# Kernel optimization log

Hardware: AMD Instinct MI355X
Metric: run time of the kernel (lower is better)

## Reference

```python
import jax, jax.numpy as jnp
import numpy as np


def setup_inputs() -> dict:
    key = jax.random.key(0)
    k1, k2 = jax.random.split(key)
    n, g, dim, cb_size = 32768, 4, 128, 512
    x = jax.random.normal(k1, (n, g, dim), dtype=jnp.float32)
    code_book = jax.random.normal(k2, (g, cb_size, dim), dtype=jnp.float32)
    return {"x": x, "code_book": code_book}


def reference(x, code_book):
    # x: (n, g, dim); code_book: (g, cb_size, dim)
    x2 = jnp.sum(x * x, axis=-1, keepdims=True)          # (n, g, 1)
    cb2 = jnp.sum(code_book * code_book, axis=-1)        # (g, cb_size)
    cross = jnp.einsum('gkd,ngd->ngk', code_book, x)     # (n, g, cb_size)
    dist = x2 + cb2 - 2.0 * cross                        # (n, g, cb_size)
    index = jnp.argmin(dist, axis=-1, keepdims=True)     # (n, g, 1) int
    one_hot = jax.nn.one_hot(index[..., 0], code_book.shape[1], dtype=dist.dtype)  # (n, g, cb_size)
    x_hat = jnp.einsum('ngk,gkd->ngd', one_hot, code_book)  # (n, g, dim)
    return (x_hat, one_hot, index)
```

## Files before the change

kernel.cpp:

```cpp
#include <hip/hip_runtime.h>
#include <hip/hip_bf16.h>

#define N_TOT 32768
#define G 4
#define DIM 128
#define CB 512
#define BM 32

#define XHAT_OFF   0
#define ONEHOT_OFF ((size_t)N_TOT * G * DIM)
#define IDX_OFF    (ONEHOT_OFF + (size_t)N_TOT * G * CB)

#define CB2_BYTES    ((size_t)G * CB * 4)
#define CBH_OFF      CB2_BYTES
#define CBHALF_BYTES ((size_t)G * CB * DIM * 2)
#define CBL_OFF      (CBH_OFF + CBHALF_BYTES)
#define WS_NEED      (CBL_OFF + CBHALF_BYTES)

typedef _Float16 half8    __attribute__((ext_vector_type(8)));
typedef _Float16 half4    __attribute__((ext_vector_type(4)));
typedef float    floatx16 __attribute__((ext_vector_type(16)));
typedef float    floatx4  __attribute__((ext_vector_type(4)));

__device__ __forceinline__ void split8(floatx4 v0, floatx4 v1, half8& hi, half8& lo) {
    float f[8] = {v0.x, v0.y, v0.z, v0.w, v1.x, v1.y, v1.z, v1.w};
#pragma unroll
    for (int e = 0; e < 8; ++e) {
        _Float16 h = (_Float16)f[e];
        hi[e] = h;
        lo[e] = (_Float16)(f[e] - (float)h);
    }
}

__global__ void cvq_cb2_kernel(const float* __restrict__ cb, float* __restrict__ cb2h) {
    int i = blockIdx.x * 256 + threadIdx.x;
    if (i >= G * CB) return;
    const float4* p = (const float4*)&cb[(size_t)i * DIM];
    float s = 0.f;
#pragma unroll
    for (int j = 0; j < DIM / 4; ++j) {
        float4 v = p[j];
        s += v.x * v.x + v.y * v.y + v.z * v.z + v.w * v.w;
    }
    cb2h[i] = 0.5f * s;
}

__global__ void cvq_cbpack_kernel(const float* __restrict__ cb,
                                  _Float16* __restrict__ cbfh, _Float16* __restrict__ cbfl) {
    int t = blockIdx.x * 256 + threadIdx.x;
    int col    = t & 31;
    int h      = (t >> 5) & 1;
    int ks     = (t >> 6) & 7;
    int colblk = (t >> 9) & 15;
    int g      = t >> 13;
    const float* src = &cb[((size_t)(g * CB + colblk * 32 + col)) * DIM + ks * 16 + h * 8];
    half8 hi, lo;
    split8(*(const floatx4*)src, *(const floatx4*)(src + 4), hi, lo);
    *(half8*)&cbfh[(size_t)t * 8] = hi;
    *(half8*)&cbfl[(size_t)t * 8] = lo;
}

__global__ __launch_bounds__(256, 3) void cvq_main_packed_kernel(
        const float* __restrict__ x,
        const _Float16* __restrict__ cbfh, const _Float16* __restrict__ cbfl,
        const float* __restrict__ cb, const float* __restrict__ cb2h,
        float* __restrict__ out) {

    __shared__ float xs[BM * DIM];
    __shared__ float part_v[4][BM];
    __shared__ int   part_i[4][BM];
    __shared__ int   idxs[BM];

    const int n0   = blockIdx.x * BM;
    const int g    = blockIdx.y;
    const int tid  = threadIdx.x;
    const int wid  = tid >> 6;
    const int lane = tid & 63;
    const int col  = lane & 31;
    const int h    = lane >> 5;

#pragma unroll
    for (int p = 0; p < 4; ++p) {
        int t = tid + p * 256;
        int r = t >> 5;
        int c = t & 31;
        floatx4 v = *(const floatx4*)&x[(((size_t)(n0 + r)) * G + g) * DIM + (c << 2)];
        *(floatx4*)&xs[r * DIM + ((c ^ (r & 7)) << 2)] = v;
    }
    __syncthreads();

    const size_t cb_base = ((size_t)g * 16 + wid * 4) * 4096 + (size_t)lane * 8;

    floatx16 acc[4] = {};

#pragma unroll
    for (int ks = 0; ks < 8; ++ks) {
        const int c0 = ks * 4 + h * 2;
        const int base = col * DIM;
        const int s = col & 7;
        floatx4 xa = *(const floatx4*)&xs[base + ((c0 ^ s) << 2)];
        floatx4 xb = *(const floatx4*)&xs[base + (((c0 + 1) ^ s) << 2)];
        half8 ah, al;
        split8(xa, xb, ah, al);
#pragma unroll
        for (int t = 0; t < 4; ++t) {
            const size_t o = cb_base + (size_t)t * 4096 + ks * 512;
            half8 bh = *(const half8*)&cbfh[o];
            half8 bl = *(const half8*)&cbfl[o];
            acc[t] = __builtin_amdgcn_mfma_f32_32x32x16_f16(ah, bh, acc[t], 0, 0, 0);
            acc[t] = __builtin_amdgcn_mfma_f32_32x32x16_f16(ah, bl, acc[t], 0, 0, 0);
            acc[t] = __builtin_amdgcn_mfma_f32_32x32x16_f16(al, bh, acc[t], 0, 0, 0);
        }
    }

    float c2v[4];
#pragma unroll
    for (int t = 0; t < 4; ++t)
        c2v[t] = cb2h[g * CB + wid * 128 + t * 32 + col];

#pragma unroll
    for (int r = 0; r < 16; ++r) {
        const int row = (r & 3) + 8 * (r >> 2) + 4 * h;
        float bv = c2v[0] - acc[0][r];
        int   bi = wid * 128 + col;
#pragma unroll
        for (int t = 1; t < 4; ++t) {
            float sc = c2v[t] - acc[t][r];
            int   kk = wid * 128 + t * 32 + col;
            if (sc < bv) { bv = sc; bi = kk; }
        }
#pragma unroll
        for (int off = 1; off < 32; off <<= 1) {
            float ov = __shfl_xor(bv, off);
            int   oi = __shfl_xor(bi, off);
            if (ov < bv || (ov == bv && oi < bi)) { bv = ov; bi = oi; }
        }
        if (col == 0) { part_v[wid][row] = bv; part_i[wid][row] = bi; }
    }
    __syncthreads();

    if (tid < BM) {
        float bv = part_v[0][tid];
        int   bi = part_i[0][tid];
#pragma unroll
        for (int w = 1; w < 4; ++w) {
            float pv = part_v[w][tid];
            int   pi = part_i[w][tid];
            if (pv < bv || (pv == bv && pi < bi)) { bv = pv; bi = pi; }
        }
        idxs[tid] = bi;
        out[IDX_OFF + (size_t)(n0 + tid) * G + g] = (float)bi;
    }
    __syncthreads();

    float* out_xhat = out + XHAT_OFF;
    float* out_oh   = out + ONEHOT_OFF;

#pragma unroll
    for (int p = 0; p < 4; ++p) {
        int t  = tid + p * 256;
        int r  = t >> 5;
        int d4 = (t & 31) << 2;
        int k  = idxs[r];
        floatx4 v = *(const floatx4*)&cb[((size_t)g * CB + k) * DIM + d4];
        __builtin_nontemporal_store(v, (floatx4*)&out_xhat[(((size_t)(n0 + r)) * G + g) * DIM + d4]);
    }

#pragma unroll
    for (int p = 0; p < 16; ++p) {
        int t  = tid + p * 256;
        int r  = t >> 7;
        int k4 = (t & 127) << 2;
        int k  = idxs[r];
        floatx4 v;
        v.x = (k4 + 0 == k) ? 1.f : 0.f;
        v.y = (k4 + 1 == k) ? 1.f : 0.f;
        v.z = (k4 + 2 == k) ? 1.f : 0.f;
        v.w = (k4 + 3 == k) ? 1.f : 0.f;
        __builtin_nontemporal_store(v, (floatx4*)&out_oh[(((size_t)(n0 + r)) * G + g) * CB + k4]);
    }
}

#define FBM 64
__global__ __launch_bounds__(256, 2) void cvq_main_kernel(
        const float* __restrict__ x,
        const float* __restrict__ cb,
        const float* __restrict__ cb2h,
        float* __restrict__ out) {

    __shared__ float part_v[4][FBM];
    __shared__ int   part_i[4][FBM];
    __shared__ int   idxs[FBM];

    const int n0   = blockIdx.x * FBM;
    const int g    = blockIdx.y;
    const int tid  = threadIdx.x;
    const int wid  = tid >> 6;
    const int lane = tid & 63;
    const int col  = lane & 31;
    const int h    = lane >> 5;
    const int klo  = h * 8;

    const float* xr0 = &x[(((size_t)(n0 + col)) * G + g) * DIM + klo];
    const float* xr1 = &x[(((size_t)(n0 + 32 + col)) * G + g) * DIM + klo];
    const float* cbr[4];
#pragma unroll
    for (int t = 0; t < 4; ++t)
        cbr[t] = &cb[((size_t)g * CB + wid * 128 + t * 32 + col) * DIM + klo];

    floatx16 acc[2][4] = {};

#pragma unroll
    for (int ks = 0; ks < 8; ++ks) {
        const int d = ks * 16;
        half8 ah[2], al[2];
        split8(*(const floatx4*)(xr0 + d), *(const floatx4*)(xr0 + d + 4), ah[0], al[0]);
        split8(*(const floatx4*)(xr1 + d), *(const floatx4*)(xr1 + d + 4), ah[1], al[1]);
#pragma unroll
        for (int t = 0; t < 4; ++t) {
            half8 bh, bl;
            split8(*(const floatx4*)(cbr[t] + d), *(const floatx4*)(cbr[t] + d + 4), bh, bl);
#pragma unroll
            for (int mt = 0; mt < 2; ++mt) {
                acc[mt][t] = __builtin_amdgcn_mfma_f32_32x32x16_f16(ah[mt], bh, acc[mt][t], 0, 0, 0);
                acc[mt][t] = __builtin_amdgcn_mfma_f32_32x32x16_f16(ah[mt], bl, acc[mt][t], 0, 0, 0);
                acc[mt][t] = __builtin_amdgcn_mfma_f32_32x32x16_f16(al[mt], bh, acc[mt][t], 0, 0, 0);
            }
        }
    }

    float c2v[4];
#pragma unroll
    for (int t = 0; t < 4; ++t)
        c2v[t] = cb2h[g * CB + wid * 128 + t * 32 + col];

#pragma unroll
    for (int mt = 0; mt < 2; ++mt) {
#pragma unroll
        for (int r = 0; r < 16; ++r) {
            const int row = mt * 32 + (r & 3) + 8 * (r >> 2) + 4 * h;
            float bv = c2v[0] - acc[mt][0][r];
            int   bi = wid * 128 + col;
#pragma unroll
            for (int t = 1; t < 4; ++t) {
                float sc = c2v[t] - acc[mt][t][r];
                int   kk = wid * 128 + t * 32 + col;
                if (sc < bv) { bv = sc; bi = kk; }
            }
#pragma unroll
            for (int off = 1; off < 32; off <<= 1) {
                float ov = __shfl_xor(bv, off);
                int   oi = __shfl_xor(bi, off);
                if (ov < bv || (ov == bv && oi < bi)) { bv = ov; bi = oi; }
            }
            if (col == 0) { part_v[wid][row] = bv; part_i[wid][row] = bi; }
        }
    }
    __syncthreads();

    if (tid < FBM) {
        float bv = part_v[0][tid];
        int   bi = part_i[0][tid];
#pragma unroll
        for (int w = 1; w < 4; ++w) {
            float pv = part_v[w][tid];
            int   pi = part_i[w][tid];
            if (pv < bv || (pv == bv && pi < bi)) { bv = pv; bi = pi; }
        }
        idxs[tid] = bi;
        out[IDX_OFF + (size_t)(n0 + tid) * G + g] = (float)bi;
    }
    __syncthreads();

    float* out_xhat = out + XHAT_OFF;
    float* out_oh   = out + ONEHOT_OFF;

#pragma unroll
    for (int p = 0; p < 8; ++p) {
        int t  = tid + p * 256;
        int r  = t >> 5;
        int d4 = (t & 31) << 2;
        int k  = idxs[r];
        floatx4 v = *(const floatx4*)&cb[((size_t)g * CB + k) * DIM + d4];
        __builtin_nontemporal_store(v, (floatx4*)&out_xhat[(((size_t)(n0 + r)) * G + g) * DIM + d4]);
    }

#pragma unroll
    for (int p = 0; p < 32; ++p) {
        int t  = tid + p * 256;
        int r  = t >> 7;
        int k4 = (t & 127) << 2;
        int k  = idxs[r];
        floatx4 v;
        v.x = (k4 + 0 == k) ? 1.f : 0.f;
        v.y = (k4 + 1 == k) ? 1.f : 0.f;
        v.z = (k4 + 2 == k) ? 1.f : 0.f;
        v.w = (k4 + 3 == k) ? 1.f : 0.f;
        __builtin_nontemporal_store(v, (floatx4*)&out_oh[(((size_t)(n0 + r)) * G + g) * CB + k4]);
    }
}

extern "C" void kernel_launch(void* const* d_in, const int* in_sizes, int n_in,
                              void* d_out, int out_size, void* d_ws, size_t ws_size,
                              hipStream_t stream) {
    const float* x  = (const float*)d_in[0];
    const float* cb = (const float*)d_in[1];
    float* out = (float*)d_out;
    char*  ws  = (char*)d_ws;
    float* cb2h = (float*)ws;

    if (ws_size >= WS_NEED) {
        _Float16* cbfh = (_Float16*)(ws + CBH_OFF);
        _Float16* cbfl = (_Float16*)(ws + CBL_OFF);
        cvq_cb2_kernel<<<dim3((G * CB + 255) / 256), dim3(256), 0, stream>>>(cb, cb2h);
        cvq_cbpack_kernel<<<dim3(G * CB * 16 / 256), dim3(256), 0, stream>>>(cb, cbfh, cbfl);
        cvq_main_packed_kernel<<<dim3(N_TOT / BM, G), dim3(256), 0, stream>>>(x, cbfh, cbfl, cb, cb2h, out);
    } else {
        cvq_cb2_kernel<<<dim3((G * CB + 255) / 256), dim3(256), 0, stream>>>(cb, cb2h);
        cvq_main_kernel<<<dim3(N_TOT / FBM, G), dim3(256), 0, stream>>>(x, cb, cb2h, out);
    }
}
```

Baseline: 154.6 us.

## Split codebook columns across eight waves per block instead of four

The main packed kernel now runs 512 threads (8 waves) per 32-row block, and each wave covers 64 codebook entries with 2 MFMA accumulators instead of 128 entries with 4. The goal is more wave-level parallelism and lower per-wave register pressure, so more MFMA work can be in flight and latency is better hidden. The cost is that each x fragment is split to fp16 hi/lo twice as often across the block, and the argmin reduction combines eight partial results instead of four.

Result: slower. 163.6 us (+5.8%).

```diff
diff --git a/kernel.cpp b/kernel.cpp
--- a/kernel.cpp
+++ b/kernel.cpp
@@ -18,7 +18,6 @@
 #define WS_NEED      (CBL_OFF + CBHALF_BYTES)
 
 typedef _Float16 half8    __attribute__((ext_vector_type(8)));
-typedef _Float16 half4    __attribute__((ext_vector_type(4)));
 typedef float    floatx16 __attribute__((ext_vector_type(16)));
 typedef float    floatx4  __attribute__((ext_vector_type(4)));
 
@@ -60,15 +59,15 @@
     *(half8*)&cbfl[(size_t)t * 8] = lo;
 }
 
-__global__ __launch_bounds__(256, 3) void cvq_main_packed_kernel(
+__global__ __launch_bounds__(512, 4) void cvq_main8w_kernel(
         const float* __restrict__ x,
         const _Float16* __restrict__ cbfh, const _Float16* __restrict__ cbfl,
         const float* __restrict__ cb, const float* __restrict__ cb2h,
         float* __restrict__ out) {
 
-    __shared__ float xs[BM * DIM];
-    __shared__ float part_v[4][BM];
-    __shared__ int   part_i[4][BM];
+    __shared__ float xstage[BM * DIM];
+    __shared__ float part_v[8][BM];
+    __shared__ int   part_i[8][BM];
     __shared__ int   idxs[BM];
 
     const int n0   = blockIdx.x * BM;
@@ -80,30 +79,30 @@
     const int h    = lane >> 5;
 
 #pragma unroll
-    for (int p = 0; p < 4; ++p) {
-        int t = tid + p * 256;
+    for (int p = 0; p < 2; ++p) {
+        int t = tid + p * 512;
         int r = t >> 5;
         int c = t & 31;
         floatx4 v = *(const floatx4*)&x[(((size_t)(n0 + r)) * G + g) * DIM + (c << 2)];
-        *(floatx4*)&xs[r * DIM + ((c ^ (r & 7)) << 2)] = v;
-    }
-    __syncthreads();
-
-    const size_t cb_base = ((size_t)g * 16 + wid * 4) * 4096 + (size_t)lane * 8;
-
-    floatx16 acc[4] = {};
+        *(floatx4*)&xstage[r * DIM + ((c ^ (r & 7)) << 2)] = v;
+    }
+    __syncthreads();
+
+    const size_t cb_base = ((size_t)g * 16 + wid * 2) * 4096 + (size_t)lane * 8;
+
+    floatx16 acc[2] = {};
 
 #pragma unroll
     for (int ks = 0; ks < 8; ++ks) {
         const int c0 = ks * 4 + h * 2;
-        const int base = col * DIM;
-        const int s = col & 7;
-        floatx4 xa = *(const floatx4*)&xs[base + ((c0 ^ s) << 2)];
-        floatx4 xb = *(const floatx4*)&xs[base + (((c0 + 1) ^ s) << 2)];
+        const int s  = col & 7;
+        const float* xb = &xstage[col * DIM];
+        floatx4 xa = *(const floatx4*)&xb[((c0 ^ s) << 2)];
+        floatx4 xc = *(const floatx4*)&xb[(((c0 + 1) ^ s) << 2)];
         half8 ah, al;
-        split8(xa, xb, ah, al);
-#pragma unroll
-        for (int t = 0; t < 4; ++t) {
+        split8(xa, xc, ah, al);
+#pragma unroll
+        for (int t = 0; t < 2; ++t) {
             const size_t o = cb_base + (size_t)t * 4096 + ks * 512;
             half8 bh = *(const half8*)&cbfh[o];
             half8 bl = *(const half8*)&cbfl[o];
@@ -113,22 +112,17 @@
         }
     }
 
-    float c2v[4];
-#pragma unroll
-    for (int t = 0; t < 4; ++t)
-        c2v[t] = cb2h[g * CB + wid * 128 + t * 32 + col];
+    const float c2v0 = cb2h[g * CB + wid * 64 + col];
+    const float c2v1 = cb2h[g * CB + wid * 64 + 32 + col];
 
 #pragma unroll
     for (int r = 0; r < 16; ++r) {
         const int row = (r & 3) + 8 * (r >> 2) + 4 * h;
-        float bv = c2v[0] - acc[0][r];
-        int   bi = wid * 128 + col;
-#pragma unroll
-        for (int t = 1; t < 4; ++t) {
-            float sc = c2v[t] - acc[t][r];
-            int   kk = wid * 128 + t * 32 + col;
-            if (sc < bv) { bv = sc; bi = kk; }
-        }
+        float bv = c2v0 - acc[0][r];
+        int   bi = wid * 64 + col;
+        float s1 = c2v1 - acc[1][r];
+        int   k1 = wid * 64 + 32 + col;
+        if (s1 < bv) { bv = s1; bi = k1; }
 #pragma unroll
         for (int off = 1; off < 32; off <<= 1) {
             float ov = __shfl_xor(bv, off);
@@ -143,7 +137,7 @@
         float bv = part_v[0][tid];
         int   bi = part_i[0][tid];
 #pragma unroll
-        for (int w = 1; w < 4; ++w) {
+        for (int w = 1; w < 8; ++w) {
             float pv = part_v[w][tid];
             int   pi = part_i[w][tid];
             if (pv < bv || (pv == bv && pi < bi)) { bv = pv; bi = pi; }
@@ -157,8 +151,8 @@
     float* out_oh   = out + ONEHOT_OFF;
 
 #pragma unroll
-    for (int p = 0; p < 4; ++p) {
-        int t  = tid + p * 256;
+    for (int p = 0; p < 2; ++p) {
+        int t  = tid + p * 512;
         int r  = t >> 5;
         int d4 = (t & 31) << 2;
         int k  = idxs[r];
@@ -167,8 +161,8 @@
     }
 
 #pragma unroll
-    for (int p = 0; p < 16; ++p) {
-        int t  = tid + p * 256;
+    for (int p = 0; p < 8; ++p) {
+        int t  = tid + p * 512;
         int r  = t >> 7;
         int k4 = (t & 127) << 2;
         int k  = idxs[r];
@@ -314,7 +308,7 @@
         _Float16* cbfl = (_Float16*)(ws + CBL_OFF);
         cvq_cb2_kernel<<<dim3((G * CB + 255) / 256), dim3(256), 0, stream>>>(cb, cb2h);
         cvq_cbpack_kernel<<<dim3(G * CB * 16 / 256), dim3(256), 0, stream>>>(cb, cbfh, cbfl);
-        cvq_main_packed_kernel<<<dim3(N_TOT / BM, G), dim3(256), 0, stream>>>(x, cbfh, cbfl, cb, cb2h, out);
+        cvq_main8w_kernel<<<dim3(N_TOT / BM, G), dim3(512), 0, stream>>>(x, cbfh, cbfl, cb, cb2h, out);
     } else {
         cvq_cb2_kernel<<<dim3((G * CB + 255) / 256), dim3(256), 0, stream>>>(cb, cb2h);
         cvq_main_kernel<<<dim3(N_TOT / FBM, G), dim3(256), 0, stream>>>(x, cb, cb2h, out);
```
